# Performance work log

Hardware: AMD Instinct MI355X
Metric: run time of the kernel (lower is better)

Reference implementation:

```python
import jax, jax.numpy as jnp
import numpy as np

# ---- static config (matches init_kwargs) ----
B, S, D = 2, 4096, 1024          # batch, seq_len, dim_input
L, ST = 512, 64                  # segment_len, state_len
H = 8                            # num_heads
DK0, DV0, DK1, DV1 = 64, 64, 64, 64  # per-head key/value dims for 2 memory levels
DH = 4096                        # dim_hidden (MLP)
T = 2 * ST + L                   # tokens per segment block: [state, segment, state]


def setup_inputs() -> dict:
    key = jax.random.key(0)
    ks = jax.random.split(key, 18)
    f32 = jnp.float32
    def w(k, shape, fan_in):
        return (jax.random.normal(k, shape, dtype=f32) / np.float32(np.sqrt(fan_in)))
    return {
        "x": jax.random.normal(ks[0], (B, S, D), dtype=f32),
        "state_init": 0.02 * jax.random.normal(ks[1], (ST, D), dtype=f32),
        # level-0 projections: dim_input -> per-head (key/value)
        "Wq0": w(ks[2], (D, H, DK0), D),
        "Wk0": w(ks[3], (D, H, DK0), D),
        "Wv0": w(ks[4], (D, H, DV0), D),
        # level-1 projections: level-0 value dim -> per-head (key/value)
        "Wq1": w(ks[5], (H, DV0, DK1), DV0),
        "Wk1": w(ks[6], (H, DV0, DK1), DV0),
        "Wv1": w(ks[7], (H, DV0, DV1), DV0),
        # output projection back to dim_input
        "Wo": w(ks[8], (H, DV1, D), H * DV1),
        "bo": jnp.zeros((D,), f32),
        "g_attn": jnp.ones((D,), f32),
        "b_attn": jnp.zeros((D,), f32),
        "W1": w(ks[9], (D, DH), D),
        "b1": jnp.zeros((DH,), f32),
        "W2": w(ks[10], (DH, D), DH),
        "b2": jnp.zeros((D,), f32),
        "g_mlp": jnp.ones((D,), f32),
        "b_mlp": jnp.zeros((D,), f32),
    }


def _layernorm(x, g, b, eps=1e-5):
    mu = jnp.mean(x, axis=-1, keepdims=True)
    var = jnp.mean(jnp.square(x - mu), axis=-1, keepdims=True)
    return (x - mu) * jax.lax.rsqrt(var + eps) * g + b


def _rope(x, pos):
    # x: (B, H, T, dk); rotary embedding with base 10000
    dk = x.shape[-1]
    inv_freq = jnp.power(jnp.float32(10000.0), -jnp.arange(0, dk, 2, dtype=jnp.float32) / dk)
    ang = pos[:, None] * inv_freq[None, :]              # (T, dk/2)
    cos, sin = jnp.cos(ang), jnp.sin(ang)
    x1, x2 = x[..., 0::2], x[..., 1::2]
    r1 = x1 * cos - x2 * sin
    r2 = x1 * sin + x2 * cos
    return jnp.stack([r1, r2], axis=-1).reshape(x.shape)


def _attend(q, k, v, mask):
    # q,k: (B,H,T,dk); v: (B,H,T,dv); causal mask (T,T)
    scale = jnp.float32(1.0 / np.sqrt(q.shape[-1]))
    scores = jnp.einsum('bhqc,bhkc->bhqk', q, k) * scale
    scores = jnp.where(mask, scores, jnp.float32(-1e30))
    p = jax.nn.softmax(scores, axis=-1)
    return jnp.einsum('bhqk,bhkv->bhqv', p, v)


def _remmtas(x, state_init, Wq0, Wk0, Wv0, Wq1, Wk1, Wv1, Wo, bo):
    b, s, d = x.shape
    n_seg = s // L
    xs = x.reshape(b, n_seg, L, d).transpose(1, 0, 2, 3)   # (n_seg, B, L, D)
    mask = jnp.tril(jnp.ones((T, T), dtype=bool))
    pos = jnp.arange(T, dtype=jnp.float32)
    state0 = jnp.broadcast_to(state_init, (b, ST, d))

    def step(state, seg):
        toks = jnp.concatenate([state, seg, state], axis=1)      # (B, T, D)
        # memory level 0
        q0 = _rope(jnp.einsum('btd,dhk->bhtk', toks, Wq0), pos)
        k0 = _rope(jnp.einsum('btd,dhk->bhtk', toks, Wk0), pos)
        v0 = jnp.einsum('btd,dhv->bhtv', toks, Wv0)
        o0 = _attend(q0, k0, v0, mask)                           # (B,H,T,DV0)
        # memory level 1 (consumes level-0 values, per-head)
        q1 = _rope(jnp.einsum('bhtv,hvk->bhtk', o0, Wq1), pos)
        k1 = _rope(jnp.einsum('bhtv,hvk->bhtk', o0, Wk1), pos)
        v1 = jnp.einsum('bhtv,hvw->bhtw', o0, Wv1)
        o1 = _attend(q1, k1, v1, mask)                           # (B,H,T,DV1)
        out = jnp.einsum('bhtv,hvd->btd', o1, Wo) + bo           # (B,T,D)
        new_state = out[:, ST + L:]                              # trailing state tokens
        return new_state, out[:, ST:ST + L]                      # segment output

    _, outs = jax.lax.scan(step, state0, xs)                     # (n_seg, B, L, D)
    return outs.transpose(1, 0, 2, 3).reshape(b, s, d)


def reference(x, state_init, Wq0, Wk0, Wv0, Wq1, Wk1, Wv1, Wo, bo,
              g_attn, b_attn, W1, b1, W2, b2, g_mlp, b_mlp):
    a = _remmtas(x, state_init, Wq0, Wk0, Wv0, Wq1, Wk1, Wv1, Wo, bo)
    h = _layernorm(a + x, g_attn, b_attn)
    m = jax.nn.gelu(h @ W1 + b1, approximate=False) @ W2 + b2
    # note: second residual adds the ORIGINAL x, per the source code
    return _layernorm(m + x, g_mlp, b_mlp)
```

## Files before the change

kernel.cpp:

```cpp
#include <hip/hip_runtime.h>
#include <hip/hip_bf16.h>

typedef __hip_bfloat16 bf16;
typedef short bf16x8 __attribute__((ext_vector_type(8)));
typedef float f32x4 __attribute__((ext_vector_type(4)));

#define CB 2
#define CS 4096
#define CD 1024
#define CL 512
#define CST 64
#define CH 8
#define CT 640
#define CDH 4096
#define NSEG 8
#define MCH 2048
#define LP 80

__device__ __forceinline__ float tof(float x) { return x; }
__device__ __forceinline__ float tof(bf16 x) { return __bfloat162float(x); }
__device__ __forceinline__ void storev(float* p, float v) { *p = v; }
__device__ __forceinline__ void storev(bf16* p, float v) { *p = __float2bfloat16(v); }

__device__ __forceinline__ float ldin(const void* p, size_t i, int f32w) {
    if (f32w) return ((const float*)p)[i];
    return __bfloat162float(((const bf16*)p)[i]);
}

__global__ void sniff_kernel(const void* x, int* flag) {
    if (threadIdx.x == 0 && blockIdx.x == 0) {
        const bf16* hb = (const bf16*)x;
        int plaus = 0;
        for (int i = 0; i < 256; ++i) {
            float v = __bfloat162float(hb[2 * i]);
            float a = fabsf(v);
            if (v == 0.f || (a > 1e-4f && a < 100.f)) ++plaus;
        }
        flag[0] = (plaus < 128) ? 1 : 0;
    }
}

__global__ __launch_bounds__(256) void transpose_kernel(
    const void* __restrict__ in, bf16* __restrict__ out, int R, int C,
    const int* __restrict__ flag)
{
    const int f32w = flag[0];
    __shared__ short t[64][72];
    int tid = threadIdx.x;
    int c0 = blockIdx.x * 64, r0 = blockIdx.y * 64;
    int cc = tid & 63, rr = tid >> 6;
#pragma unroll
    for (int i = 0; i < 16; ++i) {
        bf16 v = __float2bfloat16(ldin(in, (size_t)(r0 + rr + i * 4) * C + c0 + cc, f32w));
        t[rr + i * 4][cc] = *(short*)&v;
    }
    __syncthreads();
#pragma unroll
    for (int i = 0; i < 16; ++i)
        ((short*)out)[(size_t)(c0 + rr + i * 4) * R + r0 + cc] = t[cc][rr + i * 4];
}

__global__ __launch_bounds__(256) void transposeH_kernel(
    const void* __restrict__ Wq1, const void* __restrict__ Wk1, const void* __restrict__ Wv1,
    bf16* __restrict__ oq, bf16* __restrict__ ok, bf16* __restrict__ ov,
    const int* __restrict__ flag)
{
    const int f32w = flag[0];
    int which = blockIdx.x >> 3, hh = blockIdx.x & 7;
    const void* in = (which == 0) ? Wq1 : (which == 1) ? Wk1 : Wv1;
    bf16* out = (which == 0) ? oq : (which == 1) ? ok : ov;
    __shared__ short t[64][72];
    int tid = threadIdx.x;
    int cc = tid & 63, rr = tid >> 6;
    size_t base = (size_t)hh * 4096;
#pragma unroll
    for (int i = 0; i < 16; ++i) {
        bf16 v = __float2bfloat16(ldin(in, base + (size_t)(rr + i * 4) * 64 + cc, f32w));
        t[rr + i * 4][cc] = *(short*)&v;
    }
    __syncthreads();
#pragma unroll
    for (int i = 0; i < 16; ++i)
        ((short*)out)[base + (size_t)(rr + i * 4) * 64 + cc] = t[cc][rr + i * 4];
}

template <typename TC, int ACT, int OUTM>
__global__ __launch_bounds__(256) void mfma_lds(
    const bf16* __restrict__ A,
    const bf16* __restrict__ Bt0, const bf16* __restrict__ Bt1, const bf16* __restrict__ Bt2,
    TC* __restrict__ C0, TC* __restrict__ C1, TC* __restrict__ C2,
    const void* __restrict__ bias, int M, int N, int K, int seg,
    const int* __restrict__ flag)
{
    const int f32w = flag[0];
    const bf16* Bt = (blockIdx.z == 0) ? Bt0 : (blockIdx.z == 1 ? Bt1 : Bt2);
    TC* C = (blockIdx.z == 0) ? C0 : (blockIdx.z == 1 ? C1 : C2);

    __shared__ __align__(16) short As[128 * 64];
    __shared__ __align__(16) short Bs[128 * 64];

    const int tid = threadIdx.x;
    const int lane = tid & 63;
    const int w = tid >> 6;
    const int wm = w >> 1, wn = w & 1;
    const int gx = (int)gridDim.x;
    const int nblk = gx * (int)gridDim.y;
    const int lin = (int)blockIdx.x + (int)blockIdx.y * gx;
    const int qn = nblk >> 3;
    const int swz = (lin & 7) * qn + (lin >> 3);
    const int bm = (swz % gx) * 128, bn = (swz / gx) * 128;

    f32x4 acc[4][4];
#pragma unroll
    for (int i = 0; i < 4; ++i)
#pragma unroll
        for (int j = 0; j < 4; ++j) acc[i][j] = (f32x4){0.f, 0.f, 0.f, 0.f};

    bf16x8 rA[4], rB[4];
#pragma unroll
    for (int i = 0; i < 4; ++i) {
        int c = i * 256 + tid;
        int row = c >> 3, kc = c & 7;
        rA[i] = *(const bf16x8*)(A + (size_t)(bm + row) * K + kc * 8);
        rB[i] = *(const bf16x8*)(Bt + (size_t)(bn + row) * K + kc * 8);
    }

    for (int k0 = 0; k0 < K; k0 += 64) {
        __syncthreads();
#pragma unroll
        for (int i = 0; i < 4; ++i) {
            *(bf16x8*)&As[(size_t)(i * 256 + tid) * 8] = rA[i];
            *(bf16x8*)&Bs[(size_t)(i * 256 + tid) * 8] = rB[i];
        }
        if (k0 + 64 < K) {
            int kn = k0 + 64;
#pragma unroll
            for (int i = 0; i < 4; ++i) {
                int c = i * 256 + tid;
                int row = c >> 3, kc = c & 7;
                rA[i] = *(const bf16x8*)(A + (size_t)(bm + row) * K + kn + kc * 8);
                rB[i] = *(const bf16x8*)(Bt + (size_t)(bn + row) * K + kn + kc * 8);
            }
        }
        __syncthreads();

#pragma unroll
        for (int kh = 0; kh < 2; ++kh) {
            bf16x8 av[4], bv[4];
#pragma unroll
            for (int mi = 0; mi < 4; ++mi) {
                int r = wm * 64 + mi * 16 + (lane & 15);
                int cl = kh * 4 + (lane >> 4);
                av[mi] = *(const bf16x8*)&As[r * 64 + cl * 8];
            }
#pragma unroll
            for (int nj = 0; nj < 4; ++nj) {
                int r = wn * 64 + nj * 16 + (lane & 15);
                int cl = kh * 4 + (lane >> 4);
                bv[nj] = *(const bf16x8*)&Bs[r * 64 + cl * 8];
            }
#pragma unroll
            for (int mi = 0; mi < 4; ++mi)
#pragma unroll
                for (int nj = 0; nj < 4; ++nj)
                    acc[mi][nj] = __builtin_amdgcn_mfma_f32_16x16x32_bf16(
                        av[mi], bv[nj], acc[mi][nj], 0, 0, 0);
        }
    }

#pragma unroll
    for (int mi = 0; mi < 4; ++mi) {
#pragma unroll
        for (int nj = 0; nj < 4; ++nj) {
            int c = bn + wn * 64 + nj * 16 + (lane & 15);
            float bia = bias ? ldin(bias, c, f32w) : 0.f;
#pragma unroll
            for (int r = 0; r < 4; ++r) {
                int row = bm + wm * 64 + mi * 16 + (lane >> 4) * 4 + r;
                float v = acc[mi][nj][r] + bia;
                if (ACT == 1) v = 0.5f * v * (1.0f + erff(v * 0.70710678118654752f));
                if (OUTM == 0) {
                    storev(C + (size_t)row * N + c, v);
                } else {
                    int bb2 = row / CT, t = row % CT;
                    if (t >= CST) {
                        if (t < CST + CL)
                            storev(C0 + ((size_t)bb2 * CS + (size_t)seg * CL + (t - CST)) * CD + c, v);
                        else
                            storev(C1 + ((size_t)bb2 * CST + (t - CST - CL)) * CD + c, v);
                    }
                }
            }
        }
    }
}

__global__ __launch_bounds__(256) void ropeV_kernel(
    bf16* __restrict__ q, bf16* __restrict__ k,
    const bf16* __restrict__ v, bf16* __restrict__ vt)
{
    int t0 = blockIdx.x * 64, hh = blockIdx.y, b = blockIdx.z;
    int tid = threadIdx.x;
    __shared__ short lt[64][72];
    int c = tid & 63;
    int r0 = tid >> 6;
    int ip = c >> 1;
    float inv = powf(10000.f, -(float)(2 * ip) / 64.f);
#pragma unroll
    for (int i = 0; i < 16; ++i) {
        int r = r0 + i * 4;
        int t = t0 + r;
        size_t idx = ((size_t)b * CT + t) * 512 + hh * 64 + c;
        float qv = tof(q[idx]);
        float kv = tof(k[idx]);
        float ang = (float)t * inv;
        float sn, cs;
        sincosf(ang, &sn, &cs);
        float qp = __shfl_xor(qv, 1);
        float kp = __shfl_xor(kv, 1);
        float rq, rk;
        if (c & 1) { rq = qp * sn + qv * cs; rk = kp * sn + kv * cs; }
        else       { rq = qv * cs - qp * sn; rk = kv * cs - kp * sn; }
        q[idx] = __float2bfloat16(rq);
        k[idx] = __float2bfloat16(rk);
        lt[r][c] = ((const short*)v)[idx];
    }
    __syncthreads();
#pragma unroll
    for (int i = 0; i < 16; ++i) {
        int c2 = r0 + i * 4;
        int r2 = c;
        ((short*)vt)[((size_t)(b * CH + hh) * 64 + c2) * CT + t0 + r2] = lt[r2][c2];
    }
}

template <int FUSE>
__global__ __launch_bounds__(256) void attn_mfma(
    const bf16* __restrict__ q, const bf16* __restrict__ k, const bf16* __restrict__ vt,
    bf16* __restrict__ o,
    int qsb, int qsh, int qst,
    int ksb, int ksh, int kst,
    int ob, int oh, int ot,
    const bf16* __restrict__ Wq1t, const bf16* __restrict__ Wk1t, const bf16* __restrict__ Wv1t,
    bf16* __restrict__ q1o, bf16* __restrict__ k1o, bf16* __restrict__ v1to)
{
    const int tid = threadIdx.x;
    const int lane = tid & 63;
    const int wrow = tid >> 6;
    const int hh = blockIdx.y, b = blockIdx.z;
    const int qbase = ((int)gridDim.x - 1 - (int)blockIdx.x) * 64;

    __shared__ __align__(16) short Qs[64 * LP];
    __shared__ __align__(16) short Ks[64 * LP];
    __shared__ __align__(16) short Vs[64 * LP];
    __shared__ __align__(16) short Ps[64 * LP];

    const size_t qb0 = (size_t)b * qsb + (size_t)hh * qsh;
    const size_t kb0 = (size_t)b * ksb + (size_t)hh * ksh;
    const size_t vtb = (size_t)(b * CH + hh) * 64 * CT;

    int srow[2], skc[2], soff[2];
#pragma unroll
    for (int i = 0; i < 2; ++i) {
        int c = i * 256 + tid;
        srow[i] = c >> 3;
        skc[i] = c & 7;
        soff[i] = srow[i] * LP + skc[i] * 8;
    }

    bf16x8 rQ[2], rK[2], rV[2];
#pragma unroll
    for (int i = 0; i < 2; ++i) {
        rQ[i] = *(const bf16x8*)(q + qb0 + (size_t)(qbase + srow[i]) * qst + skc[i] * 8);
        rK[i] = *(const bf16x8*)(k + kb0 + (size_t)srow[i] * kst + skc[i] * 8);
        rV[i] = *(const bf16x8*)(vt + vtb + (size_t)srow[i] * CT + skc[i] * 8);
    }

    float mrow[4], lrow[4];
    f32x4 oacc[4];
#pragma unroll
    for (int r = 0; r < 4; ++r) { mrow[r] = -1e30f; lrow[r] = 0.f; }
#pragma unroll
    for (int nd = 0; nd < 4; ++nd) oacc[nd] = (f32x4){0.f, 0.f, 0.f, 0.f};

    const int ntiles = qbase / 64 + 1;
    for (int ti = 0; ti < ntiles; ++ti) {
        __syncthreads();
        if (ti == 0) {
#pragma unroll
            for (int i = 0; i < 2; ++i) *(bf16x8*)&Qs[soff[i]] = rQ[i];
        }
#pragma unroll
        for (int i = 0; i < 2; ++i) {
            *(bf16x8*)&Ks[soff[i]] = rK[i];
            *(bf16x8*)&Vs[soff[i]] = rV[i];
        }
        if (ti + 1 < ntiles) {
            int j1 = (ti + 1) * 64;
#pragma unroll
            for (int i = 0; i < 2; ++i) {
                rK[i] = *(const bf16x8*)(k + kb0 + (size_t)(j1 + srow[i]) * kst + skc[i] * 8);
                rV[i] = *(const bf16x8*)(vt + vtb + (size_t)srow[i] * CT + j1 + skc[i] * 8);
            }
        }
        __syncthreads();

        f32x4 sacc[4];
#pragma unroll
        for (int nj = 0; nj < 4; ++nj) sacc[nj] = (f32x4){0.f, 0.f, 0.f, 0.f};
#pragma unroll
        for (int kh = 0; kh < 2; ++kh) {
            int cl = kh * 4 + (lane >> 4);
            bf16x8 av = *(const bf16x8*)&Qs[(wrow * 16 + (lane & 15)) * LP + cl * 8];
#pragma unroll
            for (int nj = 0; nj < 4; ++nj) {
                bf16x8 bv = *(const bf16x8*)&Ks[(nj * 16 + (lane & 15)) * LP + cl * 8];
                sacc[nj] = __builtin_amdgcn_mfma_f32_16x16x32_bf16(av, bv, sacc[nj], 0, 0, 0);
            }
        }

        const bool diag = (ti == ntiles - 1);
        float pm[4] = {-1e30f, -1e30f, -1e30f, -1e30f};
#pragma unroll
        for (int nj = 0; nj < 4; ++nj) {
            int col_l = nj * 16 + (lane & 15);
#pragma unroll
            for (int r = 0; r < 4; ++r) {
                int row_l = wrow * 16 + ((lane >> 4) << 2) + r;
                float s = (diag && col_l > row_l) ? -1e30f : sacc[nj][r] * 0.125f;
                sacc[nj][r] = s;
                pm[r] = fmaxf(pm[r], s);
            }
        }
#pragma unroll
        for (int msk = 1; msk < 16; msk <<= 1)
#pragma unroll
            for (int r = 0; r < 4; ++r) pm[r] = fmaxf(pm[r], __shfl_xor(pm[r], msk));

        float corr[4], rs[4] = {0.f, 0.f, 0.f, 0.f};
#pragma unroll
        for (int r = 0; r < 4; ++r) {
            float mn = fmaxf(mrow[r], pm[r]);
            corr[r] = __expf(mrow[r] - mn);
            mrow[r] = mn;
        }
#pragma unroll
        for (int nj = 0; nj < 4; ++nj)
#pragma unroll
            for (int r = 0; r < 4; ++r) {
                float p = __expf(sacc[nj][r] - mrow[r]);
                sacc[nj][r] = p;
                rs[r] += p;
            }
#pragma unroll
        for (int msk = 1; msk < 16; msk <<= 1)
#pragma unroll
            for (int r = 0; r < 4; ++r) rs[r] += __shfl_xor(rs[r], msk);
#pragma unroll
        for (int r = 0; r < 4; ++r) lrow[r] = lrow[r] * corr[r] + rs[r];
#pragma unroll
        for (int nd = 0; nd < 4; ++nd)
#pragma unroll
            for (int r = 0; r < 4; ++r) oacc[nd][r] *= corr[r];

#pragma unroll
        for (int nj = 0; nj < 4; ++nj)
#pragma unroll
            for (int r = 0; r < 4; ++r) {
                bf16 pb = __float2bfloat16(sacc[nj][r]);
                Ps[(wrow * 16 + ((lane >> 4) << 2) + r) * LP + nj * 16 + (lane & 15)] =
                    *(short*)&pb;
            }

#pragma unroll
        for (int kh = 0; kh < 2; ++kh) {
            int cl = kh * 4 + (lane >> 4);
            bf16x8 pa = *(const bf16x8*)&Ps[(wrow * 16 + (lane & 15)) * LP + cl * 8];
#pragma unroll
            for (int nd = 0; nd < 4; ++nd) {
                bf16x8 bv = *(const bf16x8*)&Vs[(nd * 16 + (lane & 15)) * LP + cl * 8];
                oacc[nd] = __builtin_amdgcn_mfma_f32_16x16x32_bf16(pa, bv, oacc[nd], 0, 0, 0);
            }
        }
    }

    if (FUSE == 0) {
#pragma unroll
        for (int nd = 0; nd < 4; ++nd) {
#pragma unroll
            for (int r = 0; r < 4; ++r) {
                int row_g = qbase + wrow * 16 + ((lane >> 4) << 2) + r;
                int col = nd * 16 + (lane & 15);
                storev(&o[(size_t)b * ob + (size_t)hh * oh + (size_t)row_g * ot + col],
                       oacc[nd][r] / lrow[r]);
            }
        }
    } else {
#pragma unroll
        for (int nd = 0; nd < 4; ++nd)
#pragma unroll
            for (int r = 0; r < 4; ++r) {
                int row_l = wrow * 16 + ((lane >> 4) << 2) + r;
                bf16 ob16 = __float2bfloat16(oacc[nd][r] / lrow[r]);
                Qs[row_l * LP + nd * 16 + (lane & 15)] = *(short*)&ob16;
            }
        __syncthreads();

        const size_t whb = (size_t)hh * 4096;
        f32x4 qa[4], ka[4], va[4];
#pragma unroll
        for (int nj = 0; nj < 4; ++nj) {
            qa[nj] = (f32x4){0.f, 0.f, 0.f, 0.f};
            ka[nj] = (f32x4){0.f, 0.f, 0.f, 0.f};
            va[nj] = (f32x4){0.f, 0.f, 0.f, 0.f};
        }
#pragma unroll
        for (int kh = 0; kh < 2; ++kh) {
            int cl = kh * 4 + (lane >> 4);
            bf16x8 av = *(const bf16x8*)&Qs[(wrow * 16 + (lane & 15)) * LP + cl * 8];
#pragma unroll
            for (int nj = 0; nj < 4; ++nj) {
                int rowb = nj * 16 + (lane & 15);
                bf16x8 bq = *(const bf16x8*)(Wq1t + whb + (size_t)rowb * 64 + cl * 8);
                bf16x8 bk = *(const bf16x8*)(Wk1t + whb + (size_t)rowb * 64 + cl * 8);
                bf16x8 bw = *(const bf16x8*)(Wv1t + whb + (size_t)rowb * 64 + cl * 8);
                qa[nj] = __builtin_amdgcn_mfma_f32_16x16x32_bf16(av, bq, qa[nj], 0, 0, 0);
                ka[nj] = __builtin_amdgcn_mfma_f32_16x16x32_bf16(av, bk, ka[nj], 0, 0, 0);
                va[nj] = __builtin_amdgcn_mfma_f32_16x16x32_bf16(av, bw, va[nj], 0, 0, 0);
            }
        }
        const size_t bh = (size_t)(b * CH + hh);
#pragma unroll
        for (int nj = 0; nj < 4; ++nj) {
            int col = nj * 16 + (lane & 15);
            int ip = col >> 1;
            float inv = powf(10000.f, -(float)(2 * ip) / 64.f);
#pragma unroll
            for (int r = 0; r < 4; ++r) {
                int row_l = wrow * 16 + ((lane >> 4) << 2) + r;
                int t = qbase + row_l;
                float ang = (float)t * inv;
                float sn, cs;
                sincosf(ang, &sn, &cs);
                float aq = qa[nj][r], ak = ka[nj][r];
                float pq = __shfl_xor(aq, 1);
                float pk = __shfl_xor(ak, 1);
                float rq, rk;
                if (col & 1) { rq = pq * sn + aq * cs; rk = pk * sn + ak * cs; }
                else         { rq = aq * cs - pq * sn; rk = ak * cs - pk * sn; }
                size_t roff = (bh * CT + t) * 64 + col;
                q1o[roff] = __float2bfloat16(rq);
                k1o[roff] = __float2bfloat16(rk);
                v1to[(bh * 64 + col) * CT + t] = __float2bfloat16(va[nj][r]);
            }
        }
    }
}

__global__ __launch_bounds__(256) void build_toks_kernel(
    const void* __restrict__ x, const float* __restrict__ state, bf16* __restrict__ toks,
    int seg, const int* __restrict__ flag)
{
    const int f32w = flag[0];
    int idx = blockIdx.x * 256 + threadIdx.x;
    int d = idx & (CD - 1);
    int t = (idx >> 10) % CT;
    int b = idx / (CT * CD);
    float v;
    if (t < CST) v = state[(b * CST + t) * CD + d];
    else if (t < CST + CL) v = ldin(x, ((size_t)b * CS + seg * CL + (t - CST)) * CD + d, f32w);
    else v = state[(b * CST + (t - CST - CL)) * CD + d];
    toks[idx] = __float2bfloat16(v);
}

__global__ __launch_bounds__(256) void init_state_kernel(
    const void* __restrict__ s0, float* __restrict__ state, const int* __restrict__ flag)
{
    const int f32w = flag[0];
    int idx = blockIdx.x * 256 + threadIdx.x;
    state[idx] = ldin(s0, idx % (CST * CD), f32w);
}

__global__ __launch_bounds__(256) void ln_kernel(
    const float* __restrict__ ra, const void* __restrict__ x,
    const void* __restrict__ g, const void* __restrict__ bb,
    void* __restrict__ outp, int out_ext, const int* __restrict__ flag)
{
    const int f32w = flag[0];
    int row = blockIdx.x;
    int tid = threadIdx.x;
    __shared__ float buf[CD];
    __shared__ float red[4];

    float s = 0.f;
    for (int c = tid; c < CD; c += 256) {
        float v = ra[(size_t)row * CD + c] + ldin(x, (size_t)row * CD + c, f32w);
        buf[c] = v;
        s += v;
    }
#pragma unroll
    for (int off = 32; off; off >>= 1) s += __shfl_xor(s, off);
    if ((tid & 63) == 0) red[tid >> 6] = s;
    __syncthreads();
    float mu = (red[0] + red[1] + red[2] + red[3]) * (1.f / CD);
    __syncthreads();

    float vs = 0.f;
    for (int c = tid; c < CD; c += 256) {
        float d0 = buf[c] - mu;
        vs += d0 * d0;
    }
#pragma unroll
    for (int off = 32; off; off >>= 1) vs += __shfl_xor(vs, off);
    if ((tid & 63) == 0) red[tid >> 6] = vs;
    __syncthreads();
    float var = (red[0] + red[1] + red[2] + red[3]) * (1.f / CD);
    float rs = rsqrtf(var + 1e-5f);

    for (int c = tid; c < CD; c += 256) {
        float y = (buf[c] - mu) * rs * ldin(g, c, f32w) + ldin(bb, c, f32w);
        size_t idx = (size_t)row * CD + c;
        if (!out_ext) {
            ((bf16*)outp)[idx] = __float2bfloat16(y);
        } else if (f32w) {
            ((float*)outp)[idx] = y;
        } else {
            ((bf16*)outp)[idx] = __float2bfloat16(y);
        }
    }
}

extern "C" void kernel_launch(void* const* d_in, const int* in_sizes, int n_in,
                              void* d_out, int out_size, void* d_ws, size_t ws_size,
                              hipStream_t stream)
{
    const void* x      = d_in[0];
    const void* s0     = d_in[1];
    const void* Wq0    = d_in[2];
    const void* Wk0    = d_in[3];
    const void* Wv0    = d_in[4];
    const void* Wq1    = d_in[5];
    const void* Wk1    = d_in[6];
    const void* Wv1    = d_in[7];
    const void* Wo     = d_in[8];
    const void* bo     = d_in[9];
    const void* g_attn = d_in[10];
    const void* b_attn = d_in[11];
    const void* W1     = d_in[12];
    const void* b1     = d_in[13];
    const void* W2     = d_in[14];
    const void* b2     = d_in[15];
    const void* g_mlp  = d_in[16];
    const void* b_mlp  = d_in[17];

    int* flag = (int*)d_ws;
    float* f = (float*)((char*)d_ws + 16);
    float* toks_slot = f; f += (size_t)CB * CT * CD;
    float* q0_slot = f;  f += (size_t)CB * CH * CT * 64;
    float* k0_slot = f;  f += (size_t)CB * CH * CT * 64;
    float* v0_slot = f;  f += (size_t)CB * CH * CT * 64;
    float* o0_slot = f;  f += (size_t)CB * CH * CT * 64;
    float* q1_slot = f;  f += (size_t)CB * CH * CT * 64;
    float* k1_slot = f;  f += (size_t)CB * CH * CT * 64;
    float* v1_slot = f;  f += (size_t)CB * CH * CT * 64;
    float* o1t_slot = f; f += (size_t)CB * CT * (CH * 64);
    float* seg_slot = f; f += (size_t)CB * CT * CD;
    float* state = f;   f += (size_t)CB * CST * CD;
    float* a = f;       f += (size_t)CB * CS * CD;
    bf16* h = (bf16*)f;
    bf16* tail = h + (size_t)CB * CS * CD;

    bf16* toks = (bf16*)toks_slot;
    bf16* q0b = (bf16*)q0_slot;
    bf16* k0b = (bf16*)k0_slot;
    bf16* v0b = (bf16*)v0_slot;
    bf16* v0t = (bf16*)o0_slot;
    bf16* q1b = (bf16*)q1_slot;
    bf16* k1b = (bf16*)k1_slot;
    bf16* v1t = (bf16*)v1_slot;
    bf16* o1t = (bf16*)o1t_slot;
    bf16* WtQ = h;
    bf16* WtK = WtQ + (size_t)512 * 1024;
    bf16* WtV = WtK + (size_t)512 * 1024;
    bf16* WtO = WtV + (size_t)512 * 1024;
    bf16* WtQ1 = WtO + (size_t)1024 * 512;
    bf16* WtK1 = WtQ1 + (size_t)8 * 4096;
    bf16* WtV1 = WtK1 + (size_t)8 * 4096;
    bf16* g1  = (bf16*)toks_slot;
    bf16* Wt1 = g1 + (size_t)MCH * CDH;
    bf16* Wt2 = tail;

    sniff_kernel<<<1, 64, 0, stream>>>(x, flag);
    init_state_kernel<<<(CB * CST * CD) / 256, 256, 0, stream>>>(s0, state, flag);

    transpose_kernel<<<dim3(8, 16), 256, 0, stream>>>(Wq0, WtQ, CD, 512, flag);
    transpose_kernel<<<dim3(8, 16), 256, 0, stream>>>(Wk0, WtK, CD, 512, flag);
    transpose_kernel<<<dim3(8, 16), 256, 0, stream>>>(Wv0, WtV, CD, 512, flag);
    transpose_kernel<<<dim3(16, 8), 256, 0, stream>>>(Wo, WtO, 512, CD, flag);
    transposeH_kernel<<<24, 256, 0, stream>>>(Wq1, Wk1, Wv1, WtQ1, WtK1, WtV1, flag);

    for (int seg = 0; seg < NSEG; ++seg) {
        build_toks_kernel<<<(CB * CT * CD) / 256, 256, 0, stream>>>(x, state, toks, seg, flag);
        mfma_lds<bf16, 0, 0><<<dim3(10, 4, 3), 256, 0, stream>>>(
            toks, WtQ, WtK, WtV, q0b, k0b, v0b, nullptr, CB * CT, 512, CD, 0, flag);
        ropeV_kernel<<<dim3(CT / 64, CH, CB), 256, 0, stream>>>(q0b, k0b, v0b, v0t);
        attn_mfma<1><<<dim3(CT / 64, CH, CB), 256, 0, stream>>>(
            q0b, k0b, v0t, nullptr,
            CT * 512, 64, 512,
            CT * 512, 64, 512,
            0, 0, 0,
            WtQ1, WtK1, WtV1, q1b, k1b, v1t);
        attn_mfma<0><<<dim3(CT / 64, CH, CB), 256, 0, stream>>>(
            q1b, k1b, v1t, o1t,
            CH * CT * 64, CT * 64, 64,
            CH * CT * 64, CT * 64, 64,
            CT * 512, 64, 512,
            nullptr, nullptr, nullptr, nullptr, nullptr, nullptr);
        mfma_lds<float, 0, 1><<<dim3(10, 8, 1), 256, 0, stream>>>(
            o1t, WtO, WtO, WtO, a, state, a, bo, CB * CT, CD, 512, seg, flag);
    }

    ln_kernel<<<CB * CS, 256, 0, stream>>>(a, x, g_attn, b_attn, h, 0, flag);

    transpose_kernel<<<dim3(CDH / 64, CD / 64), 256, 0, stream>>>(W1, Wt1, CD, CDH, flag);
    transpose_kernel<<<dim3(CD / 64, CDH / 64), 256, 0, stream>>>(W2, Wt2, CDH, CD, flag);

    for (int c = 0; c < (CB * CS) / MCH; ++c) {
        mfma_lds<bf16, 1, 0><<<dim3(MCH / 128, CDH / 128, 1), 256, 0, stream>>>(
            h + (size_t)c * MCH * CD, Wt1, Wt1, Wt1, g1, g1, g1, b1, MCH, CDH, CD, 0, flag);
        mfma_lds<float, 0, 0><<<dim3(MCH / 128, CD / 128, 1), 256, 0, stream>>>(
            g1, Wt2, Wt2, Wt2,
            a + (size_t)c * MCH * CD, a + (size_t)c * MCH * CD, a + (size_t)c * MCH * CD,
            b2, MCH, CD, CDH, 0, flag);
    }
    ln_kernel<<<CB * CS, 256, 0, stream>>>(a, x, g_mlp, b_mlp, d_out, 1, flag);
}
```

Measured before the change: 1.328 ms.

## Deepen GEMM register prefetch to two K-tiles and drop block swizzle

The MFMA GEMM now prefetches two 64-wide K tiles into registers instead of one, alternating between two register sets. This gives global loads more time to arrive before they are written to LDS. It also removes the grouped block-index swizzle in favour of direct blockIdx mapping, which may reduce L2 reuse. The extra prefetch buffers raise register pressure and assume K is a multiple of 128.

```diff
diff --git a/kernel.cpp b/kernel.cpp
--- a/kernel.cpp
+++ b/kernel.cpp
@@ -103,12 +103,7 @@
     const int lane = tid & 63;
     const int w = tid >> 6;
     const int wm = w >> 1, wn = w & 1;
-    const int gx = (int)gridDim.x;
-    const int nblk = gx * (int)gridDim.y;
-    const int lin = (int)blockIdx.x + (int)blockIdx.y * gx;
-    const int qn = nblk >> 3;
-    const int swz = (lin & 7) * qn + (lin >> 3);
-    const int bm = (swz % gx) * 128, bn = (swz / gx) * 128;
+    const int bm = blockIdx.x * 128, bn = blockIdx.y * 128;
 
     f32x4 acc[4][4];
 #pragma unroll
@@ -116,57 +111,83 @@
 #pragma unroll
         for (int j = 0; j < 4; ++j) acc[i][j] = (f32x4){0.f, 0.f, 0.f, 0.f};
 
-    bf16x8 rA[4], rB[4];
+    int srow[4], skc[4];
 #pragma unroll
     for (int i = 0; i < 4; ++i) {
         int c = i * 256 + tid;
-        int row = c >> 3, kc = c & 7;
-        rA[i] = *(const bf16x8*)(A + (size_t)(bm + row) * K + kc * 8);
-        rB[i] = *(const bf16x8*)(Bt + (size_t)(bn + row) * K + kc * 8);
-    }
-
-    for (int k0 = 0; k0 < K; k0 += 64) {
+        srow[i] = c >> 3;
+        skc[i] = (c & 7) * 8;
+    }
+
+    bf16x8 rA0[4], rB0[4], rA1[4], rB1[4];
+#pragma unroll
+    for (int i = 0; i < 4; ++i) {
+        rA0[i] = *(const bf16x8*)(A + (size_t)(bm + srow[i]) * K + skc[i]);
+        rB0[i] = *(const bf16x8*)(Bt + (size_t)(bn + srow[i]) * K + skc[i]);
+        rA1[i] = *(const bf16x8*)(A + (size_t)(bm + srow[i]) * K + 64 + skc[i]);
+        rB1[i] = *(const bf16x8*)(Bt + (size_t)(bn + srow[i]) * K + 64 + skc[i]);
+    }
+
+#define MFMA_PHASE                                                              \
+    _Pragma("unroll")                                                           \
+    for (int kh = 0; kh < 2; ++kh) {                                            \
+        bf16x8 av[4], bv[4];                                                    \
+        _Pragma("unroll")                                                       \
+        for (int mi = 0; mi < 4; ++mi) {                                        \
+            int r = wm * 64 + mi * 16 + (lane & 15);                            \
+            int cl = kh * 4 + (lane >> 4);                                      \
+            av[mi] = *(const bf16x8*)&As[r * 64 + cl * 8];                      \
+        }                                                                       \
+        _Pragma("unroll")                                                       \
+        for (int nj = 0; nj < 4; ++nj) {                                        \
+            int r = wn * 64 + nj * 16 + (lane & 15);                            \
+            int cl = kh * 4 + (lane >> 4);                                      \
+            bv[nj] = *(const bf16x8*)&Bs[r * 64 + cl * 8];                      \
+        }                                                                       \
+        _Pragma("unroll")                                                       \
+        for (int mi = 0; mi < 4; ++mi)                                          \
+            _Pragma("unroll")                                                   \
+            for (int nj = 0; nj < 4; ++nj)                                      \
+                acc[mi][nj] = __builtin_amdgcn_mfma_f32_16x16x32_bf16(          \
+                    av[mi], bv[nj], acc[mi][nj], 0, 0, 0);                      \
+    }
+
+    for (int k0 = 0; k0 < K; k0 += 128) {
         __syncthreads();
 #pragma unroll
         for (int i = 0; i < 4; ++i) {
-            *(bf16x8*)&As[(size_t)(i * 256 + tid) * 8] = rA[i];
-            *(bf16x8*)&Bs[(size_t)(i * 256 + tid) * 8] = rB[i];
-        }
-        if (k0 + 64 < K) {
-            int kn = k0 + 64;
+            *(bf16x8*)&As[(size_t)(i * 256 + tid) * 8] = rA0[i];
+            *(bf16x8*)&Bs[(size_t)(i * 256 + tid) * 8] = rB0[i];
+        }
+        if (k0 + 128 < K) {
+            int kn = k0 + 128;
 #pragma unroll
             for (int i = 0; i < 4; ++i) {
-                int c = i * 256 + tid;
-                int row = c >> 3, kc = c & 7;
-                rA[i] = *(const bf16x8*)(A + (size_t)(bm + row) * K + kn + kc * 8);
-                rB[i] = *(const bf16x8*)(Bt + (size_t)(bn + row) * K + kn + kc * 8);
+                rA0[i] = *(const bf16x8*)(A + (size_t)(bm + srow[i]) * K + kn + skc[i]);
+                rB0[i] = *(const bf16x8*)(Bt + (size_t)(bn + srow[i]) * K + kn + skc[i]);
             }
         }
         __syncthreads();
-
-#pragma unroll
-        for (int kh = 0; kh < 2; ++kh) {
-            bf16x8 av[4], bv[4];
-#pragma unroll
-            for (int mi = 0; mi < 4; ++mi) {
-                int r = wm * 64 + mi * 16 + (lane & 15);
-                int cl = kh * 4 + (lane >> 4);
-                av[mi] = *(const bf16x8*)&As[r * 64 + cl * 8];
-            }
-#pragma unroll
-            for (int nj = 0; nj < 4; ++nj) {
-                int r = wn * 64 + nj * 16 + (lane & 15);
-                int cl = kh * 4 + (lane >> 4);
-                bv[nj] = *(const bf16x8*)&Bs[r * 64 + cl * 8];
-            }
-#pragma unroll
-            for (int mi = 0; mi < 4; ++mi)
-#pragma unroll
-                for (int nj = 0; nj < 4; ++nj)
-                    acc[mi][nj] = __builtin_amdgcn_mfma_f32_16x16x32_bf16(
-                        av[mi], bv[nj], acc[mi][nj], 0, 0, 0);
-        }
-    }
+        MFMA_PHASE
+
+        __syncthreads();
+#pragma unroll
+        for (int i = 0; i < 4; ++i) {
+            *(bf16x8*)&As[(size_t)(i * 256 + tid) * 8] = rA1[i];
+            *(bf16x8*)&Bs[(size_t)(i * 256 + tid) * 8] = rB1[i];
+        }
+        if (k0 + 192 < K) {
+            int kn = k0 + 192;
+#pragma unroll
+            for (int i = 0; i < 4; ++i) {
+                rA1[i] = *(const bf16x8*)(A + (size_t)(bm + srow[i]) * K + kn + skc[i]);
+                rB1[i] = *(const bf16x8*)(Bt + (size_t)(bn + srow[i]) * K + kn + skc[i]);
+            }
+        }
+        __syncthreads();
+        MFMA_PHASE
+    }
+#undef MFMA_PHASE
 
 #pragma unroll
     for (int mi = 0; mi < 4; ++mi) {
```

New measurement: 1.323 ms. Within noise of the previous version (-0.4%).
